# Optimization experiments

Measured on AMD Instinct MI355X. Metric: run time of the kernel, lower is better.

Reference implementation:

```python
import jax, jax.numpy as jnp
import numpy as np
from jax import lax

RADIUS = 4
HIDDEN = 64
CORR_CH = (2 * RADIUS + 1) ** 2  # 81


def _conv3x3(x, w, b):
    # x: [B, Cin, H, W], w: [Cout, Cin, 3, 3], b: [Cout]
    y = lax.conv_general_dilated(
        x, w, window_strides=(1, 1), padding='SAME',
        dimension_numbers=('NCHW', 'OIHW', 'NCHW'))
    return y + b[None, :, None, None]


def setup_inputs() -> dict:
    key = jax.random.key(0)
    ks = jax.random.split(key, 8)
    B, C, H, W = 8, 256, 128, 128
    F1 = jax.random.normal(ks[0], (B, C, H, W), dtype=jnp.float32)
    F2 = jax.random.normal(ks[1], (B, C, H, W), dtype=jnp.float32)
    # refine_net params (PyTorch Conv2d default init scale ~ 1/sqrt(fan_in))
    def conv_init(k, cout, cin):
        bound = 1.0 / np.sqrt(cin * 9)
        kw, kb = jax.random.split(k)
        w = jax.random.uniform(kw, (cout, cin, 3, 3), jnp.float32, -bound, bound)
        b = jax.random.uniform(kb, (cout,), jnp.float32, -bound, bound)
        return w, b
    w1, b1 = conv_init(ks[2], HIDDEN, CORR_CH)
    w2, b2 = conv_init(ks[3], HIDDEN, HIDDEN)
    w3, b3 = conv_init(ks[4], 2, HIDDEN)
    return {'F1': F1, 'F2': F2, 'w1': w1, 'b1': b1, 'w2': w2, 'b2': b2,
            'w3': w3, 'b3': b3}


def local_correlation(F1, F2, radius=RADIUS):
    # Correlation volume: for each (dy, dx) in the (2r+1)^2 window,
    # corr[:, k] = sum_c F1 * roll(F2, (dy, dx)) / sqrt(C).
    C = F1.shape[1]
    scale = 1.0 / np.sqrt(C).astype(np.float32)
    corr_planes = []
    for dy in range(-radius, radius + 1):
        for dx in range(-radius, radius + 1):
            shifted = jnp.roll(F2, shift=(dy, dx), axis=(2, 3))
            corr_planes.append(jnp.sum(F1 * shifted, axis=1) * scale)
    return jnp.stack(corr_planes, axis=1)  # [B, 81, H, W]


def reference(F1, F2, w1, b1, w2, b2, w3, b3):
    corr = local_correlation(F1, F2)
    h = jax.nn.relu(_conv3x3(corr, w1, b1))
    h = jax.nn.relu(_conv3x3(h, w2, b2))
    flow = _conv3x3(h, w3, b3)  # [B, 2, H, W]
    return flow
```

## Files before the change

kernel.cpp:

```cpp
#include <hip/hip_runtime.h>

typedef _Float16 half_t;
typedef _Float16 half8 __attribute__((ext_vector_type(8)));
typedef float float4v __attribute__((ext_vector_type(4)));

constexpr int NB = 8, NC = 256, NH = 128, NW = 128;
constexpr int CORR_PAD = 96;

__global__ void prep_weights_kernel(const float* __restrict__ w1,
                                    const float* __restrict__ w2,
                                    const float* __restrict__ w3,
                                    half_t* __restrict__ Wt1,
                                    half_t* __restrict__ Wt2,
                                    half_t* __restrict__ W3t) {
  int stride = gridDim.x * blockDim.x;
  int idx0 = blockIdx.x * blockDim.x + threadIdx.x;
  for (int i = idx0; i < 64 * 968; i += stride) {
    int co = i / 968, k = i % 968;
    float v = 0.f;
    if (k < 960) {
      int chunk = k / 160, rem = k % 160;
      int kk = rem / 32, r2 = rem % 32;
      int u = r2 / 16, cil = r2 % 16;
      int kykx = kk * 2 + u, ci = chunk * 16 + cil;
      if (kykx < 9 && ci < 81) {
        int ky = kykx / 3, kx = kykx % 3;
        v = w1[((co * 81 + ci) * 3 + ky) * 3 + kx];
      }
    }
    Wt1[i] = (half_t)v;
  }
  for (int i = idx0; i < 64 * 648; i += stride) {
    int co = i / 648, k = i % 648;
    float v = 0.f;
    if (k < 640) {
      int chunk = k / 160, rem = k % 160;
      int kk = rem / 32, r2 = rem % 32;
      int u = r2 / 16, cil = r2 % 16;
      int kykx = kk * 2 + u, ci = chunk * 16 + cil;
      if (kykx < 9 && ci < 64) {
        int ky = kykx / 3, kx = kykx % 3;
        v = w2[((co * 64 + ci) * 3 + ky) * 3 + kx];
      }
    }
    Wt2[i] = (half_t)v;
  }
  for (int i = idx0; i < 2 * 576; i += stride) {
    int co = i / 576, k = i % 576;
    int kykx = k / 64, ci = k % 64;
    int ky = kykx / 3, kx = kykx % 3;
    W3t[i] = (half_t)w3[((co * 64 + ci) * 3 + ky) * 3 + kx];
  }
}

__global__ __launch_bounds__(512, 4) void corr_kernel(const float* __restrict__ F1,
                                                      const float* __restrict__ F2,
                                                      half_t* __restrict__ corr) {
  __shared__ __align__(16) half_t L[10 * 128 * 32];

  int bid = blockIdx.x;
  int b = bid & 7, y = bid >> 3;
  int tid = threadIdx.x;
  int wave = tid >> 6, lane = tid & 63;
  int q = lane >> 4, l15 = lane & 15;
  int x0w = wave * 16;

  const float* F1b = F1 + (size_t)b * (NC * NH * NW);
  const float* F2b = F2 + (size_t)b * (NC * NH * NW);

  float4v acc[9][2];
#pragma unroll
  for (int i = 0; i < 9; ++i)
#pragma unroll
    for (int j = 0; j < 2; ++j)
#pragma unroll
      for (int e = 0; e < 4; ++e) acc[i][j][e] = 0.f;

  int xB = x0w + l15;
  int bfAddr = 9 * 8192 + ((xB * 64 + q * 16) ^ ((xB & 7) << 4));
  int x1 = (x0w - 4 + l15) & 127;
  int x2 = (x0w + 12 + l15) & 127;
  int a1Off = (x1 * 64 + q * 16) ^ ((x1 & 7) << 4);
  int a2Off = (x2 * 64 + q * 16) ^ ((x2 & 7) << 4);

  int sx = tid & 127;
  int swzW = ((sx & 7) << 4);
  int rc0 = tid >> 7;

  for (int c0 = 0; c0 < NC; c0 += 32) {
    __syncthreads();
    for (int it = 0; it < 20; ++it) {
      int rc = rc0 + it * 4;
      int cg = rc & 7, r = rc >> 3;
      int gy = (r == 9) ? y : ((y - 4 + r) & 127);
      const float* sp = (r == 9 ? F1b : F2b) + (size_t)(c0 + cg * 4) * (NH * NW) + gy * NW + sx;
      float v0 = sp[0];
      float v1 = sp[NH * NW];
      float v2 = sp[2 * NH * NW];
      float v3 = sp[3 * NH * NW];
      union { half_t h[4]; unsigned long long u; } pk;
      pk.h[0] = (half_t)v0; pk.h[1] = (half_t)v1; pk.h[2] = (half_t)v2; pk.h[3] = (half_t)v3;
      int byt = r * 8192 + ((sx * 64 + cg * 8) ^ swzW);
      *(unsigned long long*)((char*)L + byt) = pk.u;
    }
    __syncthreads();

    half8 bf = *(const half8*)((const char*)L + bfAddr);
#pragma unroll
    for (int dyi = 0; dyi < 9; ++dyi) {
      int rbase = (8 - dyi) * 8192;
      half8 a1 = *(const half8*)((const char*)L + rbase + a1Off);
      half8 a2 = *(const half8*)((const char*)L + rbase + a2Off);
      acc[dyi][0] = __builtin_amdgcn_mfma_f32_16x16x32_f16(a1, bf, acc[dyi][0], 0, 0, 0);
      acc[dyi][1] = __builtin_amdgcn_mfma_f32_16x16x32_f16(a2, bf, acc[dyi][1], 0, 0, 0);
    }
  }

  half_t* pbase = corr + ((size_t)b * (NH * NW) + (size_t)y * NW + xB) * CORR_PAD;
  int top1 = l15 + 8 - 4 * q;
  int top2 = l15 - 8 - 4 * q;
#pragma unroll
  for (int dyi = 0; dyi < 9; ++dyi) {
#pragma unroll
    for (int e = 0; e < 4; ++e) {
      int d1 = top1 - e;
      if (d1 >= 0 && d1 <= 8) pbase[dyi * 9 + d1] = (half_t)(acc[dyi][0][e] * 0.0625f);
      int d2 = top2 - e;
      if (d2 >= 0 && d2 <= 8) pbase[dyi * 9 + d2] = (half_t)(acc[dyi][1][e] * 0.0625f);
    }
  }
}

template <int CIN_PAD, int NCHUNK, bool RELU>
__global__ __launch_bounds__(512, 4) void conv_kernel(const half_t* __restrict__ src,
                                                      const half_t* __restrict__ Wt,
                                                      const float* __restrict__ bias,
                                                      half_t* __restrict__ dst) {
  constexpr int KW = NCHUNK * 160 + 8;
  __shared__ __align__(16) half_t Alds[64 * 168];
  __shared__ __align__(16) half_t Btile[6 * 130 * 24];

  int bid = blockIdx.x;
  int b = bid & 7, strip = bid >> 3;
  int y0 = strip * 4;
  int tid = threadIdx.x;

  int wave = tid >> 6, lane = tid & 63;
  int row = wave >> 1;
  int xh = (wave & 1) * 64;
  int l15 = lane & 15, q = lane >> 4;

  float4v acc[4][4];
#pragma unroll
  for (int i = 0; i < 4; ++i)
#pragma unroll
    for (int j = 0; j < 4; ++j)
#pragma unroll
      for (int e = 0; e < 4; ++e) acc[i][j][e] = 0.f;

  const half_t* srcb = src + (size_t)b * NH * NW * CIN_PAD;

  for (int chunk = 0; chunk < NCHUNK; ++chunk) {
    __syncthreads();
    for (int s = tid; s < 1280; s += 512) {
      int co = s / 20, k8 = s % 20;
      *(half8*)(Alds + co * 168 + k8 * 8) =
          *(const half8*)(Wt + (size_t)co * KW + chunk * 160 + k8 * 8);
    }
    for (int s = tid; s < 1560; s += 512) {
      int sub = (s >= 780) ? 1 : 0;
      int s2 = s - sub * 780;
      int trow = s2 / 130, tcol = s2 % 130;
      int yy = y0 - 1 + trow, xx = tcol - 1;
      half8 v;
#pragma unroll
      for (int e = 0; e < 8; ++e) v[e] = (half_t)0.f;
      if (yy >= 0 && yy < NH && xx >= 0 && xx < NW)
        v = *(const half8*)(srcb + ((size_t)yy * NW + xx) * CIN_PAD + chunk * 16 + sub * 8);
      *(half8*)(Btile + ((size_t)trow * 130 + tcol) * 24 + sub * 8) = v;
    }
    __syncthreads();
#pragma unroll
    for (int kk = 0; kk < 5; ++kk) {
      half8 a[4];
#pragma unroll
      for (int mf = 0; mf < 4; ++mf)
        a[mf] = *(const half8*)(Alds + (size_t)(mf * 16 + l15) * 168 + kk * 32 + q * 8);
      int u = q >> 1, cil8 = (q & 1) * 8;
      int kykx = kk * 2 + u;
      int dy = 0, dx = 0;
      if (kykx < 9) { dy = kykx / 3 - 1; dx = kykx % 3 - 1; }
      int trow = row + 1 + dy;
      half8 bf[4];
#pragma unroll
      for (int nf = 0; nf < 4; ++nf) {
        int tcol = 1 + xh + nf * 16 + l15 + dx;
        bf[nf] = *(const half8*)(Btile + ((size_t)trow * 130 + tcol) * 24 + cil8);
      }
#pragma unroll
      for (int mf = 0; mf < 4; ++mf)
#pragma unroll
        for (int nf = 0; nf < 4; ++nf)
          acc[mf][nf] = __builtin_amdgcn_mfma_f32_16x16x32_f16(a[mf], bf[nf], acc[mf][nf], 0, 0, 0);
    }
  }

  int y = y0 + row;
  half_t* dstb = dst + ((size_t)b * NH * NW + (size_t)y * NW) * 64;
#pragma unroll
  for (int mf = 0; mf < 4; ++mf) {
    int cobase = mf * 16 + q * 4;
    float4v bv = *(const float4v*)(bias + cobase);
#pragma unroll
    for (int nf = 0; nf < 4; ++nf) {
      int x = xh + nf * 16 + l15;
      union { half_t h[4]; unsigned long long u64; } pk;
#pragma unroll
      for (int e = 0; e < 4; ++e) {
        float v = acc[mf][nf][e] + bv[e];
        if (RELU) v = v > 0.f ? v : 0.f;
        pk.h[e] = (half_t)v;
      }
      *(unsigned long long*)(dstb + (size_t)x * 64 + cobase) = pk.u64;
    }
  }
}

__global__ __launch_bounds__(256) void conv3_kernel(const half_t* __restrict__ h2,
                                                    const half_t* __restrict__ W3t,
                                                    const float* __restrict__ b3,
                                                    float* __restrict__ out) {
  __shared__ __align__(16) half_t w[2 * 576];
  __shared__ __align__(16) half_t tile[4 * 128 * 64];

  int bid = blockIdx.x;
  int b = bid & 7, y0 = (bid >> 3) * 2;
  int tid = threadIdx.x;

  for (int i = tid * 8; i < 1152; i += 256 * 8) *(half8*)(w + i) = *(const half8*)(W3t + i);

  const half_t* hb = h2 + (size_t)b * NH * NW * 64;
  for (int u = tid; u < 4096; u += 256) {
    int c8 = u & 7, x = (u >> 3) & 127, rr = u >> 10;
    int yy = y0 - 1 + rr;
    half8 v;
#pragma unroll
    for (int e = 0; e < 8; ++e) v[e] = (half_t)0.f;
    if (yy >= 0 && yy < NH) v = *(const half8*)(hb + ((size_t)yy * NW + x) * 64 + c8 * 8);
    int byt = (rr * 16384 + x * 128 + c8 * 16) ^ ((x & 7) << 4);
    *(half8*)((char*)tile + byt) = v;
  }
  __syncthreads();

  int x = tid & 127, ry = tid >> 7;
  int y = y0 + ry;
  float a0 = 0.f, a1 = 0.f;
#pragma unroll
  for (int dy = -1; dy <= 1; ++dy) {
#pragma unroll
    for (int dx = -1; dx <= 1; ++dx) {
      int xx = x + dx;
      if (xx < 0 || xx >= NW) continue;
      int kykx = (dy + 1) * 3 + (dx + 1);
      int trow = 1 + ry + dy;
#pragma unroll
      for (int c8 = 0; c8 < 8; ++c8) {
        int byt = (trow * 16384 + xx * 128 + c8 * 16) ^ ((xx & 7) << 4);
        half8 v = *(const half8*)((const char*)tile + byt);
        half8 w0 = *(const half8*)(w + kykx * 64 + c8 * 8);
        half8 w1 = *(const half8*)(w + 576 + kykx * 64 + c8 * 8);
#pragma unroll
        for (int j = 0; j < 8; ++j) {
          a0 = __builtin_fmaf((float)v[j], (float)w0[j], a0);
          a1 = __builtin_fmaf((float)v[j], (float)w1[j], a1);
        }
      }
    }
  }
  out[((size_t)b * 2 + 0) * NH * NW + (size_t)y * NW + x] = a0 + b3[0];
  out[((size_t)b * 2 + 1) * NH * NW + (size_t)y * NW + x] = a1 + b3[1];
}

extern "C" void kernel_launch(void* const* d_in, const int* in_sizes, int n_in,
                              void* d_out, int out_size, void* d_ws, size_t ws_size,
                              hipStream_t stream) {
  const float* F1 = (const float*)d_in[0];
  const float* F2 = (const float*)d_in[1];
  const float* w1 = (const float*)d_in[2];
  const float* b1 = (const float*)d_in[3];
  const float* w2 = (const float*)d_in[4];
  const float* b2 = (const float*)d_in[5];
  const float* w3 = (const float*)d_in[6];
  const float* b3 = (const float*)d_in[7];
  float* out = (float*)d_out;

  char* ws = (char*)d_ws;
  const size_t corr_bytes = (size_t)NB * NH * NW * CORR_PAD * 2;
  const size_t h_bytes = (size_t)NB * NH * NW * 64 * 2;
  const size_t h1_off = corr_bytes;
  const size_t h2_off = h1_off + h_bytes;
  const size_t wt1_off = h2_off + h_bytes;
  const size_t wt2_off = wt1_off + (size_t)64 * 968 * 2;
  const size_t w3t_off = wt2_off + (size_t)64 * 648 * 2;

  half_t* corr = (half_t*)(ws);
  half_t* h1 = (half_t*)(ws + h1_off);
  half_t* h2 = (half_t*)(ws + h2_off);
  half_t* Wt1 = (half_t*)(ws + wt1_off);
  half_t* Wt2 = (half_t*)(ws + wt2_off);
  half_t* W3t = (half_t*)(ws + w3t_off);

  hipMemsetAsync(corr, 0, corr_bytes, stream);
  prep_weights_kernel<<<128, 256, 0, stream>>>(w1, w2, w3, Wt1, Wt2, W3t);
  corr_kernel<<<1024, 512, 0, stream>>>(F1, F2, corr);
  conv_kernel<96, 6, true><<<256, 512, 0, stream>>>(corr, Wt1, b1, h1);
  conv_kernel<64, 4, true><<<256, 512, 0, stream>>>(h1, Wt2, b2, h2);
  conv3_kernel<<<512, 256, 0, stream>>>(h2, W3t, b3, out);
}
```

Before: 571.7 us.

## Restructure pipeline: NHWC F2 prepass, LDS-free corr/convs, padded layouts, MFMA conv3

Adds a prepass that converts F2 to NHWC fp16. The correlation kernel now reads F2 directly from global memory (cached) instead of staging through LDS, and drops its syncthreads. The conv kernels switch to a padded-x NHWC layout with per-row blocks and no LDS, reading weights pre-packed per (kykx, ci-slice). The final conv is rewritten to use MFMA. The memset goes away because pads are zeroed in-kernel and workspace buffers are aliased. The risk is the extra transpose pass over F2 plus heavier global and L2 traffic from removing the LDS tiles.

Result: slower. 600.1 us (+5.0%).

```diff
diff --git a/kernel.cpp b/kernel.cpp
--- a/kernel.cpp
+++ b/kernel.cpp
@@ -5,68 +5,58 @@
 typedef float float4v __attribute__((ext_vector_type(4)));
 
 constexpr int NB = 8, NC = 256, NH = 128, NW = 128;
-constexpr int CORR_PAD = 96;
+constexpr int XPAD = 130;
+constexpr int C1 = 96;
 
 __global__ void prep_weights_kernel(const float* __restrict__ w1,
                                     const float* __restrict__ w2,
                                     const float* __restrict__ w3,
-                                    half_t* __restrict__ Wt1,
-                                    half_t* __restrict__ Wt2,
-                                    half_t* __restrict__ W3t) {
+                                    half_t* __restrict__ WtX1,
+                                    half_t* __restrict__ WtX2,
+                                    half_t* __restrict__ WtX3) {
   int stride = gridDim.x * blockDim.x;
-  int idx0 = blockIdx.x * blockDim.x + threadIdx.x;
-  for (int i = idx0; i < 64 * 968; i += stride) {
-    int co = i / 968, k = i % 968;
-    float v = 0.f;
-    if (k < 960) {
-      int chunk = k / 160, rem = k % 160;
-      int kk = rem / 32, r2 = rem % 32;
-      int u = r2 / 16, cil = r2 % 16;
-      int kykx = kk * 2 + u, ci = chunk * 16 + cil;
-      if (kykx < 9 && ci < 81) {
-        int ky = kykx / 3, kx = kykx % 3;
-        v = w1[((co * 81 + ci) * 3 + ky) * 3 + kx];
-      }
-    }
-    Wt1[i] = (half_t)v;
-  }
-  for (int i = idx0; i < 64 * 648; i += stride) {
-    int co = i / 648, k = i % 648;
-    float v = 0.f;
-    if (k < 640) {
-      int chunk = k / 160, rem = k % 160;
-      int kk = rem / 32, r2 = rem % 32;
-      int u = r2 / 16, cil = r2 % 16;
-      int kykx = kk * 2 + u, ci = chunk * 16 + cil;
-      if (kykx < 9 && ci < 64) {
-        int ky = kykx / 3, kx = kykx % 3;
-        v = w2[((co * 64 + ci) * 3 + ky) * 3 + kx];
-      }
-    }
-    Wt2[i] = (half_t)v;
-  }
-  for (int i = idx0; i < 2 * 576; i += stride) {
-    int co = i / 576, k = i % 576;
-    int kykx = k / 64, ci = k % 64;
+  int i0 = blockIdx.x * blockDim.x + threadIdx.x;
+  for (int i = i0; i < 27 * 64 * 32; i += stride) {
+    int s = i >> 11, r = i & 2047, co = r >> 5, cq = r & 31;
+    int kykx = s / 3, ci = (s % 3) * 32 + cq;
     int ky = kykx / 3, kx = kykx % 3;
-    W3t[i] = (half_t)w3[((co * 64 + ci) * 3 + ky) * 3 + kx];
-  }
-}
-
-__global__ __launch_bounds__(512, 4) void corr_kernel(const float* __restrict__ F1,
-                                                      const float* __restrict__ F2,
-                                                      half_t* __restrict__ corr) {
-  __shared__ __align__(16) half_t L[10 * 128 * 32];
-
+    float v = (ci < 81) ? w1[((co * 81 + ci) * 3 + ky) * 3 + kx] : 0.f;
+    WtX1[i] = (half_t)v;
+  }
+  for (int i = i0; i < 18 * 64 * 32; i += stride) {
+    int s = i >> 11, r = i & 2047, co = r >> 5, cq = r & 31;
+    int kykx = s >> 1, ci = (s & 1) * 32 + cq;
+    int ky = kykx / 3, kx = kykx % 3;
+    WtX2[i] = (half_t)w2[((co * 64 + ci) * 3 + ky) * 3 + kx];
+  }
+  for (int i = i0; i < 18 * 16 * 32; i += stride) {
+    int s = i >> 9, r = i & 511, co = r >> 5, cq = r & 31;
+    int kykx = s >> 1, ci = (s & 1) * 32 + cq;
+    int ky = kykx / 3, kx = kykx % 3;
+    float v = (co < 2) ? w3[((co * 64 + ci) * 3 + ky) * 3 + kx] : 0.f;
+    WtX3[i] = (half_t)v;
+  }
+}
+
+__global__ __launch_bounds__(256) void nhwc_kernel(const float* __restrict__ F2,
+                                                   half_t* __restrict__ F2n) {
+  int v = blockIdx.x * 256 + threadIdx.x;
+  int x = v & 127, y = (v >> 7) & 127, cg = (v >> 14) & 31, b = v >> 19;
+  const float* sp = F2 + (((size_t)(b * NC + cg * 8) * NH + y) * NW + x);
+  half8 h;
+#pragma unroll
+  for (int j = 0; j < 8; ++j) h[j] = (half_t)sp[(size_t)j * NH * NW];
+  *(half8*)(F2n + (((size_t)(b * NH + y) * NW + x) * NC + cg * 8)) = h;
+}
+
+__global__ __launch_bounds__(512) void corr_kernel(const float* __restrict__ F1,
+                                                   const half_t* __restrict__ F2n,
+                                                   half_t* __restrict__ corr) {
   int bid = blockIdx.x;
   int b = bid & 7, y = bid >> 3;
-  int tid = threadIdx.x;
-  int wave = tid >> 6, lane = tid & 63;
+  int tid = threadIdx.x, wave = tid >> 6, lane = tid & 63;
   int q = lane >> 4, l15 = lane & 15;
-  int x0w = wave * 16;
-
-  const float* F1b = F1 + (size_t)b * (NC * NH * NW);
-  const float* F2b = F2 + (size_t)b * (NC * NH * NW);
+  int x0w = wave * 16, xB = x0w + l15;
 
   float4v acc[9][2];
 #pragma unroll
@@ -76,47 +66,31 @@
 #pragma unroll
       for (int e = 0; e < 4; ++e) acc[i][j][e] = 0.f;
 
-  int xB = x0w + l15;
-  int bfAddr = 9 * 8192 + ((xB * 64 + q * 16) ^ ((xB & 7) << 4));
+  const float* F1b = F1 + (size_t)b * NC * NH * NW + (size_t)y * NW + xB;
+  const half_t* F2b = F2n + (size_t)b * NH * NW * NC;
+
   int x1 = (x0w - 4 + l15) & 127;
   int x2 = (x0w + 12 + l15) & 127;
-  int a1Off = (x1 * 64 + q * 16) ^ ((x1 & 7) << 4);
-  int a2Off = (x2 * 64 + q * 16) ^ ((x2 & 7) << 4);
-
-  int sx = tid & 127;
-  int swzW = ((sx & 7) << 4);
-  int rc0 = tid >> 7;
+
+  int rowoff[9];
+#pragma unroll
+  for (int r = 0; r < 9; ++r) rowoff[r] = ((y - 4 + r) & 127) * NW * NC;
 
   for (int c0 = 0; c0 < NC; c0 += 32) {
-    __syncthreads();
-    for (int it = 0; it < 20; ++it) {
-      int rc = rc0 + it * 4;
-      int cg = rc & 7, r = rc >> 3;
-      int gy = (r == 9) ? y : ((y - 4 + r) & 127);
-      const float* sp = (r == 9 ? F1b : F2b) + (size_t)(c0 + cg * 4) * (NH * NW) + gy * NW + sx;
-      float v0 = sp[0];
-      float v1 = sp[NH * NW];
-      float v2 = sp[2 * NH * NW];
-      float v3 = sp[3 * NH * NW];
-      union { half_t h[4]; unsigned long long u; } pk;
-      pk.h[0] = (half_t)v0; pk.h[1] = (half_t)v1; pk.h[2] = (half_t)v2; pk.h[3] = (half_t)v3;
-      int byt = r * 8192 + ((sx * 64 + cg * 8) ^ swzW);
-      *(unsigned long long*)((char*)L + byt) = pk.u;
-    }
-    __syncthreads();
-
-    half8 bf = *(const half8*)((const char*)L + bfAddr);
+    half8 bf;
+#pragma unroll
+    for (int j = 0; j < 8; ++j) bf[j] = (half_t)F1b[(size_t)(c0 + q * 8 + j) * (NH * NW)];
 #pragma unroll
     for (int dyi = 0; dyi < 9; ++dyi) {
-      int rbase = (8 - dyi) * 8192;
-      half8 a1 = *(const half8*)((const char*)L + rbase + a1Off);
-      half8 a2 = *(const half8*)((const char*)L + rbase + a2Off);
+      const half_t* rp = F2b + rowoff[8 - dyi] + c0 + q * 8;
+      half8 a1 = *(const half8*)(rp + x1 * NC);
+      half8 a2 = *(const half8*)(rp + x2 * NC);
       acc[dyi][0] = __builtin_amdgcn_mfma_f32_16x16x32_f16(a1, bf, acc[dyi][0], 0, 0, 0);
       acc[dyi][1] = __builtin_amdgcn_mfma_f32_16x16x32_f16(a2, bf, acc[dyi][1], 0, 0, 0);
     }
   }
 
-  half_t* pbase = corr + ((size_t)b * (NH * NW) + (size_t)y * NW + xB) * CORR_PAD;
+  half_t* pbase = corr + ((size_t)(b * NH + y) * XPAD + xB + 1) * C1;
   int top1 = l15 + 8 - 4 * q;
   int top2 = l15 - 8 - 4 * q;
 #pragma unroll
@@ -129,156 +103,130 @@
       if (d2 >= 0 && d2 <= 8) pbase[dyi * 9 + d2] = (half_t)(acc[dyi][1][e] * 0.0625f);
     }
   }
-}
-
-template <int CIN_PAD, int NCHUNK, bool RELU>
-__global__ __launch_bounds__(512, 4) void conv_kernel(const half_t* __restrict__ src,
-                                                      const half_t* __restrict__ Wt,
-                                                      const float* __restrict__ bias,
-                                                      half_t* __restrict__ dst) {
-  constexpr int KW = NCHUNK * 160 + 8;
-  __shared__ __align__(16) half_t Alds[64 * 168];
-  __shared__ __align__(16) half_t Btile[6 * 130 * 24];
-
+  if (q == 0) {
+    pbase[81] = (half_t)0.f;
+#pragma unroll
+    for (int k = 0; k < 7; ++k) *(unsigned int*)((char*)pbase + 164 + 4 * k) = 0u;
+  }
+  if (tid < 48) {
+    int slot = (tid < 24) ? 0 : 129;
+    int o = tid % 24;
+    half_t* pp = corr + ((size_t)(b * NH + y) * XPAD + slot) * C1;
+    *(unsigned long long*)((char*)pp + o * 8) = 0ull;
+  }
+}
+
+template <int CIN, int KSPL, bool RELU>
+__global__ __launch_bounds__(256) void conv_kernel(const half_t* __restrict__ src,
+                                                   const half_t* __restrict__ WtX,
+                                                   const float* __restrict__ bias,
+                                                   half_t* __restrict__ dst) {
   int bid = blockIdx.x;
-  int b = bid & 7, strip = bid >> 3;
-  int y0 = strip * 4;
-  int tid = threadIdx.x;
-
-  int wave = tid >> 6, lane = tid & 63;
-  int row = wave >> 1;
-  int xh = (wave & 1) * 64;
-  int l15 = lane & 15, q = lane >> 4;
-
-  float4v acc[4][4];
-#pragma unroll
-  for (int i = 0; i < 4; ++i)
+  int b = bid & 7, y = bid >> 3;
+  int tid = threadIdx.x, w = tid >> 6, lane = tid & 63;
+  int q = lane >> 4, l15 = lane & 15;
+  int xh = (w & 1) * 64, coh = (w >> 1) * 32;
+
+  float4v acc[2][4];
+#pragma unroll
+  for (int i = 0; i < 2; ++i)
 #pragma unroll
     for (int j = 0; j < 4; ++j)
 #pragma unroll
       for (int e = 0; e < 4; ++e) acc[i][j][e] = 0.f;
 
-  const half_t* srcb = src + (size_t)b * NH * NW * CIN_PAD;
-
-  for (int chunk = 0; chunk < NCHUNK; ++chunk) {
-    __syncthreads();
-    for (int s = tid; s < 1280; s += 512) {
-      int co = s / 20, k8 = s % 20;
-      *(half8*)(Alds + co * 168 + k8 * 8) =
-          *(const half8*)(Wt + (size_t)co * KW + chunk * 160 + k8 * 8);
-    }
-    for (int s = tid; s < 1560; s += 512) {
-      int sub = (s >= 780) ? 1 : 0;
-      int s2 = s - sub * 780;
-      int trow = s2 / 130, tcol = s2 % 130;
-      int yy = y0 - 1 + trow, xx = tcol - 1;
-      half8 v;
-#pragma unroll
-      for (int e = 0; e < 8; ++e) v[e] = (half_t)0.f;
-      if (yy >= 0 && yy < NH && xx >= 0 && xx < NW)
-        v = *(const half8*)(srcb + ((size_t)yy * NW + xx) * CIN_PAD + chunk * 16 + sub * 8);
-      *(half8*)(Btile + ((size_t)trow * 130 + tcol) * 24 + sub * 8) = v;
-    }
-    __syncthreads();
-#pragma unroll
-    for (int kk = 0; kk < 5; ++kk) {
-      half8 a[4];
-#pragma unroll
-      for (int mf = 0; mf < 4; ++mf)
-        a[mf] = *(const half8*)(Alds + (size_t)(mf * 16 + l15) * 168 + kk * 32 + q * 8);
-      int u = q >> 1, cil8 = (q & 1) * 8;
-      int kykx = kk * 2 + u;
-      int dy = 0, dx = 0;
-      if (kykx < 9) { dy = kykx / 3 - 1; dx = kykx % 3 - 1; }
-      int trow = row + 1 + dy;
-      half8 bf[4];
+  const half_t* srcb = src + (size_t)(b * NH) * XPAD * CIN;
+  const half_t* wp = WtX + (coh + l15) * 32 + q * 8;
+  int xb = xh + l15 + 1;
+
+#pragma unroll
+  for (int s = 0; s < 9 * KSPL; ++s) {
+    int kykx = s / KSPL, ci0 = (s % KSPL) * 32;
+    int dy = kykx / 3 - 1, dx = kykx % 3 - 1;
+    int ty = y + dy;
+    if ((unsigned)ty < (unsigned)NH) {
+      half8 a0 = *(const half8*)(wp + s * 2048);
+      half8 a1 = *(const half8*)(wp + s * 2048 + 512);
+      const half_t* rp = srcb + (size_t)ty * XPAD * CIN + ci0 + q * 8;
 #pragma unroll
       for (int nf = 0; nf < 4; ++nf) {
-        int tcol = 1 + xh + nf * 16 + l15 + dx;
-        bf[nf] = *(const half8*)(Btile + ((size_t)trow * 130 + tcol) * 24 + cil8);
+        half8 bf = *(const half8*)(rp + (size_t)(xb + nf * 16 + dx) * CIN);
+        acc[0][nf] = __builtin_amdgcn_mfma_f32_16x16x32_f16(a0, bf, acc[0][nf], 0, 0, 0);
+        acc[1][nf] = __builtin_amdgcn_mfma_f32_16x16x32_f16(a1, bf, acc[1][nf], 0, 0, 0);
       }
-#pragma unroll
-      for (int mf = 0; mf < 4; ++mf)
-#pragma unroll
-        for (int nf = 0; nf < 4; ++nf)
-          acc[mf][nf] = __builtin_amdgcn_mfma_f32_16x16x32_f16(a[mf], bf[nf], acc[mf][nf], 0, 0, 0);
-    }
-  }
-
-  int y = y0 + row;
-  half_t* dstb = dst + ((size_t)b * NH * NW + (size_t)y * NW) * 64;
-#pragma unroll
-  for (int mf = 0; mf < 4; ++mf) {
-    int cobase = mf * 16 + q * 4;
-    float4v bv = *(const float4v*)(bias + cobase);
+    }
+  }
+
+  half_t* drow = dst + (size_t)(b * NH + y) * XPAD * 64;
+#pragma unroll
+  for (int mf = 0; mf < 2; ++mf) {
+    int co = coh + mf * 16 + q * 4;
+    float4v bv = *(const float4v*)(bias + co);
 #pragma unroll
     for (int nf = 0; nf < 4; ++nf) {
       int x = xh + nf * 16 + l15;
-      union { half_t h[4]; unsigned long long u64; } pk;
+      union { half_t h[4]; unsigned long long u; } pk;
 #pragma unroll
       for (int e = 0; e < 4; ++e) {
         float v = acc[mf][nf][e] + bv[e];
         if (RELU) v = v > 0.f ? v : 0.f;
         pk.h[e] = (half_t)v;
       }
-      *(unsigned long long*)(dstb + (size_t)x * 64 + cobase) = pk.u64;
-    }
+      *(unsigned long long*)(drow + (size_t)(x + 1) * 64 + co) = pk.u;
+    }
+  }
+  if (tid < 32) {
+    int slot = (tid < 16) ? 0 : 129;
+    int o = tid & 15;
+    *(unsigned long long*)((char*)(drow + (size_t)slot * 64) + o * 8) = 0ull;
   }
 }
 
 __global__ __launch_bounds__(256) void conv3_kernel(const half_t* __restrict__ h2,
-                                                    const half_t* __restrict__ W3t,
+                                                    const half_t* __restrict__ WtX3,
                                                     const float* __restrict__ b3,
                                                     float* __restrict__ out) {
-  __shared__ __align__(16) half_t w[2 * 576];
-  __shared__ __align__(16) half_t tile[4 * 128 * 64];
-
   int bid = blockIdx.x;
   int b = bid & 7, y0 = (bid >> 3) * 2;
-  int tid = threadIdx.x;
-
-  for (int i = tid * 8; i < 1152; i += 256 * 8) *(half8*)(w + i) = *(const half8*)(W3t + i);
-
-  const half_t* hb = h2 + (size_t)b * NH * NW * 64;
-  for (int u = tid; u < 4096; u += 256) {
-    int c8 = u & 7, x = (u >> 3) & 127, rr = u >> 10;
-    int yy = y0 - 1 + rr;
-    half8 v;
-#pragma unroll
-    for (int e = 0; e < 8; ++e) v[e] = (half_t)0.f;
-    if (yy >= 0 && yy < NH) v = *(const half8*)(hb + ((size_t)yy * NW + x) * 64 + c8 * 8);
-    int byt = (rr * 16384 + x * 128 + c8 * 16) ^ ((x & 7) << 4);
-    *(half8*)((char*)tile + byt) = v;
-  }
-  __syncthreads();
-
-  int x = tid & 127, ry = tid >> 7;
-  int y = y0 + ry;
-  float a0 = 0.f, a1 = 0.f;
-#pragma unroll
-  for (int dy = -1; dy <= 1; ++dy) {
-#pragma unroll
-    for (int dx = -1; dx <= 1; ++dx) {
-      int xx = x + dx;
-      if (xx < 0 || xx >= NW) continue;
-      int kykx = (dy + 1) * 3 + (dx + 1);
-      int trow = 1 + ry + dy;
-#pragma unroll
-      for (int c8 = 0; c8 < 8; ++c8) {
-        int byt = (trow * 16384 + xx * 128 + c8 * 16) ^ ((xx & 7) << 4);
-        half8 v = *(const half8*)((const char*)tile + byt);
-        half8 w0 = *(const half8*)(w + kykx * 64 + c8 * 8);
-        half8 w1 = *(const half8*)(w + 576 + kykx * 64 + c8 * 8);
-#pragma unroll
-        for (int j = 0; j < 8; ++j) {
-          a0 = __builtin_fmaf((float)v[j], (float)w0[j], a0);
-          a1 = __builtin_fmaf((float)v[j], (float)w1[j], a1);
-        }
+  int tid = threadIdx.x, w = tid >> 6, lane = tid & 63;
+  int q = lane >> 4, l15 = lane & 15;
+  int y = y0 + (w >> 1), xh = (w & 1) * 64;
+
+  half8 a[18];
+#pragma unroll
+  for (int s = 0; s < 18; ++s) a[s] = *(const half8*)(WtX3 + (s * 16 + l15) * 32 + q * 8);
+
+  float4v acc[4];
+#pragma unroll
+  for (int j = 0; j < 4; ++j)
+#pragma unroll
+    for (int e = 0; e < 4; ++e) acc[j][e] = 0.f;
+
+  const half_t* hb = h2 + (size_t)(b * NH) * XPAD * 64;
+#pragma unroll
+  for (int s = 0; s < 18; ++s) {
+    int kykx = s >> 1, ci0 = (s & 1) * 32;
+    int dy = kykx / 3 - 1, dx = kykx % 3 - 1;
+    int ty = y + dy;
+    if ((unsigned)ty < (unsigned)NH) {
+      const half_t* rp = hb + (size_t)ty * XPAD * 64 + ci0 + q * 8;
+#pragma unroll
+      for (int nf = 0; nf < 4; ++nf) {
+        half8 bf = *(const half8*)(rp + (size_t)(xh + nf * 16 + l15 + 1 + dx) * 64);
+        acc[nf] = __builtin_amdgcn_mfma_f32_16x16x32_f16(a[s], bf, acc[nf], 0, 0, 0);
       }
     }
   }
-  out[((size_t)b * 2 + 0) * NH * NW + (size_t)y * NW + x] = a0 + b3[0];
-  out[((size_t)b * 2 + 1) * NH * NW + (size_t)y * NW + x] = a1 + b3[1];
+
+  if (q == 0) {
+    float c0v = b3[0], c1v = b3[1];
+#pragma unroll
+    for (int nf = 0; nf < 4; ++nf) {
+      int x = xh + nf * 16 + l15;
+      out[((size_t)(b * 2 + 0) * NH + y) * NW + x] = acc[nf][0] + c0v;
+      out[((size_t)(b * 2 + 1) * NH + y) * NW + x] = acc[nf][1] + c1v;
+    }
+  }
 }
 
 extern "C" void kernel_launch(void* const* d_in, const int* in_sizes, int n_in,
@@ -295,25 +243,23 @@
   float* out = (float*)d_out;
 
   char* ws = (char*)d_ws;
-  const size_t corr_bytes = (size_t)NB * NH * NW * CORR_PAD * 2;
-  const size_t h_bytes = (size_t)NB * NH * NW * 64 * 2;
-  const size_t h1_off = corr_bytes;
-  const size_t h2_off = h1_off + h_bytes;
-  const size_t wt1_off = h2_off + h_bytes;
-  const size_t wt2_off = wt1_off + (size_t)64 * 968 * 2;
-  const size_t w3t_off = wt2_off + (size_t)64 * 648 * 2;
-
-  half_t* corr = (half_t*)(ws);
-  half_t* h1 = (half_t*)(ws + h1_off);
-  half_t* h2 = (half_t*)(ws + h2_off);
-  half_t* Wt1 = (half_t*)(ws + wt1_off);
-  half_t* Wt2 = (half_t*)(ws + wt2_off);
-  half_t* W3t = (half_t*)(ws + w3t_off);
-
-  hipMemsetAsync(corr, 0, corr_bytes, stream);
-  prep_weights_kernel<<<128, 256, 0, stream>>>(w1, w2, w3, Wt1, Wt2, W3t);
-  corr_kernel<<<1024, 512, 0, stream>>>(F1, F2, corr);
-  conv_kernel<96, 6, true><<<256, 512, 0, stream>>>(corr, Wt1, b1, h1);
-  conv_kernel<64, 4, true><<<256, 512, 0, stream>>>(h1, Wt2, b2, h2);
-  conv3_kernel<<<512, 256, 0, stream>>>(h2, W3t, b3, out);
-}
+  const size_t f2n_bytes = (size_t)NB * NH * NW * NC * 2;
+  const size_t corr_bytes = (size_t)NB * NH * XPAD * C1 * 2;
+  const size_t h_bytes = (size_t)NB * NH * XPAD * 64 * 2;
+
+  half_t* F2n = (half_t*)ws;
+  half_t* corr = (half_t*)(ws + f2n_bytes);
+  half_t* h1 = (half_t*)ws;
+  half_t* h2 = (half_t*)(ws + h_bytes);
+  char* wbase = ws + f2n_bytes + corr_bytes;
+  half_t* WtX1 = (half_t*)wbase;
+  half_t* WtX2 = (half_t*)(wbase + 110592);
+  half_t* WtX3 = (half_t*)(wbase + 110592 + 73728);
+
+  prep_weights_kernel<<<64, 256, 0, stream>>>(w1, w2, w3, WtX1, WtX2, WtX3);
+  nhwc_kernel<<<16384, 256, 0, stream>>>(F2, F2n);
+  corr_kernel<<<1024, 512, 0, stream>>>(F1, F2n, corr);
+  conv_kernel<96, 3, true><<<1024, 256, 0, stream>>>(corr, WtX1, b1, h1);
+  conv_kernel<64, 2, true><<<1024, 256, 0, stream>>>(h1, WtX2, b2, h2);
+  conv3_kernel<<<512, 256, 0, stream>>>(h2, WtX3, b3, out);
+}
```
